# Performance work log

Measured on AMD Instinct MI355X. Metric: run time of the kernel, lower is better.

## Reference

```python
import jax, jax.numpy as jnp
import numpy as np

EPS = 1e-5

def avg_pool3s2(x):
    # AvgPool2d(kernel=3, stride=2, no padding) on NCHW
    s = jax.lax.reduce_window(x, 0.0, jax.lax.add, (1, 1, 3, 3), (1, 1, 2, 2), 'VALID')
    return s / 9.0

def conv1x1(x, W):
    # x: [n,c,h,w], W: [out,c]
    return jnp.einsum('nchw,oc->nohw', x, W)

def batchnorm(x, g, b):
    # training-mode BN over (N,H,W), biased variance (matches torch normalization)
    m = x.mean(axis=(0, 2, 3), keepdims=True)
    v = x.var(axis=(0, 2, 3), keepdims=True)
    return (x - m) * jax.lax.rsqrt(v + EPS) * g[None, :, None, None] + b[None, :, None, None]

def coord_features(hp, wp):
    # [8, hp, wp]: xmin, ymin, xmax, ymax, xctr, yctr, 1/W, 1/H
    w = jnp.arange(wp, dtype=jnp.float32)
    h = jnp.arange(hp, dtype=jnp.float32)
    xmin = w / wp * 2 - 1
    xmax = (w + 1) / wp * 2 - 1
    xctr = (xmin + xmax) / 2
    ymin = h / hp * 2 - 1
    ymax = (h + 1) / hp * 2 - 1
    yctr = (ymin + ymax) / 2
    bx = lambda a: jnp.broadcast_to(a[None, :], (hp, wp))
    by = lambda a: jnp.broadcast_to(a[:, None], (hp, wp))
    const = lambda v: jnp.full((hp, wp), v, dtype=jnp.float32)
    return jnp.stack([bx(xmin), by(ymin), bx(xmax), by(ymax), bx(xctr), by(yctr),
                      const(1.0 / wp), const(1.0 / hp)], axis=0)

def resize_bilinear_ac(x, H, W):
    # bilinear upsample with align_corners=True, x: [n,c,h,w]
    h, w = x.shape[2], x.shape[3]
    ys = jnp.linspace(0.0, h - 1.0, H)
    xs = jnp.linspace(0.0, w - 1.0, W)
    y0 = jnp.floor(ys).astype(jnp.int32); y1 = jnp.minimum(y0 + 1, h - 1); wy = (ys - y0)[None, None, :, None]
    x0 = jnp.floor(xs).astype(jnp.int32); x1 = jnp.minimum(x0 + 1, w - 1); wx = (xs - x0)[None, None, None, :]
    rows = x[:, :, y0, :] * (1 - wy) + x[:, :, y1, :] * wy          # [n,c,H,w]
    return rows[:, :, :, x0] * (1 - wx) + rows[:, :, :, x1] * wx    # [n,c,H,W]

def setup_inputs() -> dict:
    key = jax.random.key(0)
    ks = jax.random.split(key, 8)
    n, in_dim, hid, h, w = 4, 256, 10, 129, 129
    d = hid + 8  # 18
    return {
        'p_fea': jax.random.normal(ks[0], (n, in_dim, h, w), dtype=jnp.float32),
        'hu': jax.random.normal(ks[1], (n, hid, h, w), dtype=jnp.float32),
        'Wq': jax.random.normal(ks[2], (d, d), dtype=jnp.float32) * 0.05,
        'Wk': jax.random.normal(ks[3], (d, in_dim + 8), dtype=jnp.float32) * 0.05,
        'Wv': jax.random.normal(ks[4], (128, in_dim), dtype=jnp.float32) * 0.05,
        'g_v': jnp.ones((128,), dtype=jnp.float32),
        'b_v': jnp.zeros((128,), dtype=jnp.float32),
        'Wp': jax.random.normal(ks[5], (hid, 128), dtype=jnp.float32) * 0.05,
        'g_p': jnp.ones((hid,), dtype=jnp.float32),
        'b_p': jnp.zeros((hid,), dtype=jnp.float32),
    }

def reference(p_fea, hu, Wq, Wk, Wv, g_v, b_v, Wp, g_p, b_p):
    n, c, h, w = p_fea.shape
    p = avg_pool3s2(p_fea)   # [n,256,hp,wp]
    u = avg_pool3s2(hu)      # [n,10,hp,wp]
    hp, wp = p.shape[2], p.shape[3]
    L = hp * wp
    coord = jnp.broadcast_to(coord_features(hp, wp)[None], (n, 8, hp, wp))
    query = conv1x1(jnp.concatenate([u, coord], axis=1), Wq).reshape(n, -1, L).transpose(0, 2, 1)  # [n,L,18]
    key_t = conv1x1(jnp.concatenate([p, coord], axis=1), Wk).reshape(n, -1, L)                      # [n,18,L]
    val = jax.nn.relu(batchnorm(conv1x1(p, Wv), g_v, b_v)).reshape(n, 128, L)                       # [n,128,L]
    energy = jnp.einsum('nlc,ncm->nlm', query, key_t)            # [n,L,L]
    attn = jax.nn.softmax(energy, axis=-1)
    ctx = jnp.einsum('ncm,nlm->ncl', val, attn).reshape(n, 128, hp, wp)
    ctx = jax.nn.relu(batchnorm(conv1x1(ctx, Wp), g_p, b_p))     # [n,10,hp,wp]
    return resize_bilinear_ac(ctx, h, w)                          # [n,10,h,w]
```

## Files before the change

### kernel.cpp

```cpp
#include <hip/hip_runtime.h>
#include <hip/hip_bf16.h>
#include <cstdint>

#define NN   4
#define LL   4096
#define DD   18
#define CVV  128
#define CIN  256
#define CUU  10
#define HH   129
#define COO  10

typedef unsigned short ushort_t;
typedef __attribute__((ext_vector_type(8))) short short8v;
typedef __attribute__((ext_vector_type(4))) short short4v;
typedef __attribute__((ext_vector_type(4))) float f32x4;

#define PB_OFF   ((size_t)0)
#define OP_OFF   ((size_t)2097152)
#define VAL_OFF  ((size_t)2260992)
#define QT_OFF   ((size_t)3309568)
#define KT_OFF   ((size_t)3571712)
#define VT_OFF   ((size_t)3833856)
#define VSC_OFF  ((size_t)4882432)
#define VSH_OFF  ((size_t)4882560)
#define S2_OFF   ((size_t)4882688)
#define SH2_OFF  ((size_t)4882704)
#define PART_OFF ((size_t)4882720)
#define PART2_OFF ((size_t)4915488)
#define KMAX_OFF ((size_t)4916768)

static __device__ __forceinline__ ushort_t f2bf(float x) {
    unsigned int u = __float_as_uint(x);
    unsigned int r = (u + 0x7fffu + ((u >> 16) & 1u)) >> 16;
    return (ushort_t)r;
}
static __device__ __forceinline__ float bf2f(ushort_t b) {
    return __uint_as_float(((unsigned int)b) << 16);
}

static __device__ __forceinline__ void gload16(const void* g, void* l) {
    __builtin_amdgcn_global_load_lds(
        (const __attribute__((address_space(1))) void*)g,
        (__attribute__((address_space(3))) void*)l, 16, 0, 0);
}

__global__ __launch_bounds__(256) void pool_bf_kernel(const float* __restrict__ src,
                                                      ushort_t* __restrict__ dst,
                                                      int* __restrict__ kz) {
    if (kz != nullptr && blockIdx.x == 0 && threadIdx.x < 128) kz[threadIdx.x] = 0;
    int b = blockIdx.x;
    int plane = b >> 4;
    int rg = b & 15;
    __shared__ float rows[9][132];
    const float* sp = src + (size_t)plane * (HH * HH) + (size_t)(rg * 8) * HH;
    #pragma unroll
    for (int j = 0; j < 9; ++j) {
        if (threadIdx.x < HH) rows[j][threadIdx.x] = sp[(size_t)j * HH + threadIdx.x];
    }
    __syncthreads();
    int row = threadIdx.x >> 6, ow = threadIdx.x & 63;
    const float* r0 = rows[2 * row];
    const float* r1 = rows[2 * row + 1];
    const float* r2 = rows[2 * row + 2];
    int x = 2 * ow;
    float sum = r0[x] + r0[x + 1] + r0[x + 2]
              + r1[x] + r1[x + 1] + r1[x + 2]
              + r2[x] + r2[x + 1] + r2[x + 2];
    dst[(size_t)plane * 4096 + (size_t)(rg * 4 + row) * 64 + ow] = f2bf(sum * (1.0f / 9.0f));
}

__global__ __launch_bounds__(256) void qk2f_kernel(const ushort_t* __restrict__ pb,
                                                   const float* __restrict__ hu,
                                                   const float* __restrict__ Wq,
                                                   const float* __restrict__ Wk,
                                                   ushort_t* __restrict__ qt,
                                                   char* __restrict__ kt_c,
                                                   int* __restrict__ kmaxb) {
    int n = blockIdx.x >> 6;
    int mb = blockIdx.x & 63;
    int tid = threadIdx.x;
    int mloc = tid & 63;
    int cs = tid >> 6;
    int m = mb * 64 + mloc;
    int hi = m >> 6, wi = m & 63;

    __shared__ float kacc[4][64][21];

    float coord[8];
    coord[0] = wi * (2.0f / 64.0f) - 1.0f;
    coord[1] = hi * (2.0f / 64.0f) - 1.0f;
    coord[2] = (wi + 1) * (2.0f / 64.0f) - 1.0f;
    coord[3] = (hi + 1) * (2.0f / 64.0f) - 1.0f;
    coord[4] = 0.5f * (coord[0] + coord[2]);
    coord[5] = 0.5f * (coord[1] + coord[3]);
    coord[6] = 1.0f / 64.0f;
    coord[7] = 1.0f / 64.0f;

    {
        float acc[DD];
        #pragma unroll
        for (int o = 0; o < DD; ++o) acc[o] = 0.0f;
        const ushort_t* pc = pb + ((size_t)(n * CIN + cs * 64)) * LL + m;
        for (int c0 = 0; c0 < 64; ++c0) {
            float pv = bf2f(pc[(size_t)c0 * LL]);
            const float* wr = Wk + (cs * 64 + c0);
            #pragma unroll
            for (int o = 0; o < DD; ++o) acc[o] = fmaf(pv, wr[o * 264], acc[o]);
        }
        if (cs == 3) {
            #pragma unroll
            for (int j = 0; j < 8; ++j) {
                float cv = coord[j];
                #pragma unroll
                for (int o = 0; o < DD; ++o) acc[o] = fmaf(cv, Wk[o * 264 + CIN + j], acc[o]);
            }
        }
        #pragma unroll
        for (int o = 0; o < DD; ++o) kacc[cs][mloc][o] = acc[o];
    }
    if (cs == 0) {
        float acc[DD];
        #pragma unroll
        for (int o = 0; o < DD; ++o) acc[o] = 0.0f;
        const float* hub = hu + ((size_t)(n * CUU)) * (HH * HH) + (size_t)(2 * hi) * HH + 2 * wi;
        for (int cq = 0; cq < CUU; ++cq) {
            const float* s = hub + (size_t)cq * (HH * HH);
            float uv = (s[0] + s[1] + s[2]
                      + s[HH] + s[HH + 1] + s[HH + 2]
                      + s[2 * HH] + s[2 * HH + 1] + s[2 * HH + 2]) * (1.0f / 9.0f);
            #pragma unroll
            for (int o = 0; o < DD; ++o) acc[o] = fmaf(uv, Wq[o * DD + cq], acc[o]);
        }
        #pragma unroll
        for (int j = 0; j < 8; ++j) {
            float cv = coord[j];
            #pragma unroll
            for (int o = 0; o < DD; ++o) acc[o] = fmaf(cv, Wq[o * DD + CUU + j], acc[o]);
        }
        union { short8v v[4]; ushort_t s[32]; } pk;
        #pragma unroll
        for (int o = 0; o < 32; ++o) pk.s[o] = (o < DD) ? f2bf(acc[o]) : (ushort_t)0;
        short8v* qrow = (short8v*)(qt + ((size_t)(n * LL) + m) * 32);
        #pragma unroll
        for (int j = 0; j < 4; ++j) qrow[j] = pk.v[j];
    }
    __syncthreads();
    {
        int j = cs;
        union { short8v v; ushort_t s[8]; } pk;
        #pragma unroll
        for (int i = 0; i < 8; ++i) {
            int o = j * 8 + i;
            float v = 0.0f;
            if (o < DD)
                v = kacc[0][mloc][o] + kacc[1][mloc][o] + kacc[2][mloc][o] + kacc[3][mloc][o];
            pk.s[i] = (o < DD) ? f2bf(v) : (ushort_t)0;
        }
        int byte = ((mloc << 6) | (j << 4)) ^ (((mloc >> 1) & 7) << 4);
        *(short8v*)(kt_c + (size_t)n * 262144 + (size_t)mb * 4096 + byte) = pk.v;

        int mb8[8];
        #pragma unroll
        for (int i = 0; i < 8; ++i) mb8[i] = (int)(pk.s[i] & 0x7fffu);
        #pragma unroll
        for (int off = 1; off < 64; off <<= 1) {
            #pragma unroll
            for (int i = 0; i < 8; ++i) {
                int ov = __shfl_xor(mb8[i], off);
                mb8[i] = max(mb8[i], ov);
            }
        }
        if (mloc == 0) {
            #pragma unroll
            for (int i = 0; i < 8; ++i)
                atomicMax(&kmaxb[n * 32 + cs * 8 + i], mb8[i] << 16);
        }
    }
}

__global__ __launch_bounds__(256, 2) void val_gemm3_kernel(const ushort_t* __restrict__ pb,
                                                           const float* __restrict__ Wv,
                                                           ushort_t* __restrict__ val,
                                                           float* __restrict__ part) {
    int b = blockIdx.x;
    int n  = b >> 7;
    int cb = (b >> 5) & 3;
    int mb = b & 31;
    int tid = threadIdx.x;
    int cg = tid >> 5;
    int mg = tid & 31;
    int ch0 = cb * 32;
    int m0 = mb * 128;

    __shared__ float Wt[256][36];

    {
        int c4 = tid & 63;
        int chq = tid >> 6;
        #pragma unroll
        for (int j = 0; j < 8; ++j) {
            int ch = chq * 8 + j;
            float4 v = *(const float4*)&Wv[(size_t)(ch0 + ch) * CIN + c4 * 4];
            Wt[c4 * 4 + 0][ch] = v.x;
            Wt[c4 * 4 + 1][ch] = v.y;
            Wt[c4 * 4 + 2][ch] = v.z;
            Wt[c4 * 4 + 3][ch] = v.w;
        }
    }
    __syncthreads();

    const ushort_t* pbb = pb + (size_t)n * CIN * LL + m0 + mg * 4;
    f32x4 a0 = {0.f,0.f,0.f,0.f}, a1 = {0.f,0.f,0.f,0.f};
    f32x4 a2 = {0.f,0.f,0.f,0.f}, a3 = {0.f,0.f,0.f,0.f};

    #pragma unroll 4
    for (int c = 0; c < CIN; ++c) {
        short4v ps = *(const short4v*)(pbb + (size_t)c * LL);
        f32x4 pv;
        pv[0] = bf2f((ushort_t)ps[0]); pv[1] = bf2f((ushort_t)ps[1]);
        pv[2] = bf2f((ushort_t)ps[2]); pv[3] = bf2f((ushort_t)ps[3]);
        f32x4 wv = *(const f32x4*)&Wt[c][cg * 4];
        a0 += pv * wv.x;
        a1 += pv * wv.y;
        a2 += pv * wv.z;
        a3 += pv * wv.w;
    }

    size_t out = ((size_t)(n * CVV + ch0 + cg * 4)) * LL + m0 + mg * 4;
    union { short4v v; ushort_t s[4]; } w0, w1, w2, w3;
    #pragma unroll
    for (int i = 0; i < 4; ++i) {
        w0.s[i] = f2bf(a0[i]); w1.s[i] = f2bf(a1[i]);
        w2.s[i] = f2bf(a2[i]); w3.s[i] = f2bf(a3[i]);
    }
    *(short4v*)&val[out]          = w0.v;
    *(short4v*)&val[out + LL]     = w1.v;
    *(short4v*)&val[out + 2*LL]   = w2.v;
    *(short4v*)&val[out + 3*LL]   = w3.v;

    float s1[4], s2[4];
    s1[0] = a0[0]+a0[1]+a0[2]+a0[3]; s2[0] = a0[0]*a0[0]+a0[1]*a0[1]+a0[2]*a0[2]+a0[3]*a0[3];
    s1[1] = a1[0]+a1[1]+a1[2]+a1[3]; s2[1] = a1[0]*a1[0]+a1[1]*a1[1]+a1[2]*a1[2]+a1[3]*a1[3];
    s1[2] = a2[0]+a2[1]+a2[2]+a2[3]; s2[2] = a2[0]*a2[0]+a2[1]*a2[1]+a2[2]*a2[2]+a2[3]*a2[3];
    s1[3] = a3[0]+a3[1]+a3[2]+a3[3]; s2[3] = a3[0]*a3[0]+a3[1]*a3[1]+a3[2]*a3[2]+a3[3]*a3[3];
    #pragma unroll
    for (int off = 1; off < 32; off <<= 1) {
        #pragma unroll
        for (int i = 0; i < 4; ++i) {
            s1[i] += __shfl_xor(s1[i], off);
            s2[i] += __shfl_xor(s2[i], off);
        }
    }
    if (mg == 0) {
        #pragma unroll
        for (int i = 0; i < 4; ++i) {
            part[(((size_t)b * 8 + cg) * 4 + i) * 2]     = s1[i];
            part[(((size_t)b * 8 + cg) * 4 + i) * 2 + 1] = s2[i];
        }
    }
}

__global__ __launch_bounds__(128) void bn_finalize_v_kernel(const float* __restrict__ part,
                                                            const float* __restrict__ g,
                                                            const float* __restrict__ bta,
                                                            float* __restrict__ scale,
                                                            float* __restrict__ shift) {
    int ch = threadIdx.x;
    if (ch >= CVV) return;
    int cb = ch >> 5;
    int cg = (ch & 31) >> 2;
    int i = ch & 3;
    float s1 = 0.0f, s2 = 0.0f;
    for (int n = 0; n < NN; ++n) {
        for (int mb = 0; mb < 32; ++mb) {
            int b = n * 128 + cb * 32 + mb;
            size_t idx = (((size_t)b * 8 + cg) * 4 + i) * 2;
            s1 += part[idx];
            s2 += part[idx + 1];
        }
    }
    float mean = s1 * (1.0f / (NN * LL));
    float var = s2 * (1.0f / (NN * LL)) - mean * mean;
    float inv = rsqrtf(var + 1e-5f);
    float sc = g[ch] * inv;
    scale[ch] = sc;
    shift[ch] = bta[ch] - mean * sc;
}

__global__ __launch_bounds__(256) void bn_apply2_kernel(const ushort_t* __restrict__ val,
                                                        const float* __restrict__ scale,
                                                        const float* __restrict__ shift,
                                                        char* __restrict__ vt_c) {
    int t = blockIdx.x * 256 + threadIdx.x;
    int mq = t & 511;
    int ch = (t >> 9) & 127;
    int n = t >> 16;
    int m0 = mq * 8;
    short8v vs = *(const short8v*)(val + ((size_t)(n * CVV + ch)) * LL + m0);
    float sc = scale[ch], sh = shift[ch];
    union { short8v v; ushort_t s[8]; } pk;
    #pragma unroll
    for (int i = 0; i < 8; ++i)
        pk.s[i] = f2bf(fmaxf(fmaf(bf2f((ushort_t)vs[i]), sc, sh), 0.0f));
    int tile = m0 >> 6, mloc = m0 & 63;
    size_t byte = (size_t)n * 1048576 + (size_t)tile * 16384
                + (size_t)(((ch << 7) | (mloc << 1)) ^ ((ch & 7) << 4));
    *(short8v*)(vt_c + byte) = pk.v;
}

struct PW { ushort_t p[16][72]; };

__global__ __launch_bounds__(256, 2) void attn_proj_kernel(const ushort_t* __restrict__ qt,
                                                           const char* __restrict__ kt_c,
                                                           const char* __restrict__ vt_c,
                                                           const int* __restrict__ kmaxb,
                                                           const float* __restrict__ Wp,
                                                           float* __restrict__ ypart,
                                                           float* __restrict__ Lp) {
    int orig = blockIdx.x;
    int bid = ((orig & 7) << 6) | (orig >> 3);
    int qb = bid & 63;
    int sM = (bid >> 6) & 1;
    int n = bid >> 7;
    int tid = threadIdx.x;
    int w = tid >> 6, lane = tid & 63, c = lane & 15, g = lane >> 4;
    int l0w = qb * 64 + w * 16;

    __shared__ __align__(16) ushort_t K_t[2][2048];
    __shared__ __align__(16) ushort_t V_t[2][8192];
    __shared__ PW pws[4];
    __shared__ float Wpl[COO][CVV];

    for (int i = tid; i < COO * CVV; i += 256) Wpl[i >> 7][i & 127] = Wp[i];

    const char* ktb = kt_c + (size_t)n * 262144;
    const char* vtb = vt_c + (size_t)n * 1048576;
    int tk64 = sM * 32;

    short8v qf = *(const short8v*)(qt + (((size_t)n * LL + l0w + c) << 5) + g * 8);
    int vxor = (c & 7) << 4;

    float bound = 0.0f;
    {
        const int* km = kmaxb + n * 32 + g * 8;
        #pragma unroll
        for (int i = 0; i < 8; ++i) {
            float kv = __int_as_float(km[i]);
            float aq = __uint_as_float(((unsigned int)((ushort_t)qf[i]) & 0x7fffu) << 16);
            bound = fmaf(aq, kv, bound);
        }
        bound += __shfl_xor(bound, 16);
        bound += __shfl_xor(bound, 32);
    }
    float M[4];
    #pragma unroll
    for (int r = 0; r < 4; ++r) M[r] = __shfl(bound, g * 4 + r);

    f32x4 O[8];
    #pragma unroll
    for (int i = 0; i < 8; ++i) O[i] = (f32x4){0.f, 0.f, 0.f, 0.f};
    float Lacc[4] = {0.f, 0.f, 0.f, 0.f};

    {
        const char* ks = ktb + (size_t)tk64 * 4096 + w * 1024 + lane * 16;
        gload16(ks, (char*)K_t[0] + w * 1024);
        const char* vs = vtb + (size_t)tk64 * 16384 + w * 4096 + lane * 16;
        #pragma unroll
        for (int i = 0; i < 4; ++i)
            gload16(vs + i * 1024, (char*)V_t[0] + w * 4096 + i * 1024);
    }
    __syncthreads();
    int buf = 0;
    for (int mt = 0; mt < 32; ++mt) {
        if (mt + 1 < 32) {
            const char* ks = ktb + (size_t)(tk64 + mt + 1) * 4096 + w * 1024 + lane * 16;
            gload16(ks, (char*)K_t[buf ^ 1] + w * 1024);
            const char* vs = vtb + (size_t)(tk64 + mt + 1) * 16384 + w * 4096 + lane * 16;
            #pragma unroll
            for (int i = 0; i < 4; ++i)
                gload16(vs + i * 1024, (char*)V_t[buf ^ 1] + w * 4096 + i * 1024);
        }
        f32x4 S[4];
        const char* kb = (const char*)K_t[buf];
        #pragma unroll
        for (int t = 0; t < 4; ++t) {
            int krow = t * 16 + c;
            int kby = ((krow << 6) | (g << 4)) ^ (((krow >> 1) & 7) << 4);
            short8v kf = *(const short8v*)(kb + kby);
            S[t] = __builtin_amdgcn_mfma_f32_16x16x32_bf16(qf, kf, (f32x4){0.f, 0.f, 0.f, 0.f}, 0, 0, 0);
        }
        #pragma unroll
        for (int t = 0; t < 4; ++t) {
            #pragma unroll
            for (int r = 0; r < 4; ++r) {
                float pv = __expf(S[t][r] - M[r]);
                Lacc[r] += pv;
                pws[w].p[g * 4 + r][t * 16 + c] = f2bf(pv);
            }
        }
        short8v pa0 = *(const short8v*)&pws[w].p[c][g * 8];
        short8v pa1 = *(const short8v*)&pws[w].p[c][32 + g * 8];
        const char* vb = (const char*)V_t[buf];
        __builtin_amdgcn_s_setprio(1);
        #pragma unroll
        for (int ct = 0; ct < 8; ++ct) {
            int row = ct * 16 + c;
            int vby0 = (row << 7) | ((g << 4) ^ vxor);
            int vby1 = (row << 7) | (((1 << 6) | (g << 4)) ^ vxor);
            short8v v0 = *(const short8v*)(vb + vby0);
            short8v v1 = *(const short8v*)(vb + vby1);
            O[ct] = __builtin_amdgcn_mfma_f32_16x16x32_bf16(pa0, v0, O[ct], 0, 0, 0);
            O[ct] = __builtin_amdgcn_mfma_f32_16x16x32_bf16(pa1, v1, O[ct], 0, 0, 0);
        }
        __builtin_amdgcn_s_setprio(0);
        __syncthreads();
        buf ^= 1;
    }
    #pragma unroll
    for (int off = 1; off < 16; off <<= 1) {
        #pragma unroll
        for (int r = 0; r < 4; ++r) Lacc[r] += __shfl_xor(Lacc[r], off);
    }

    float yp[COO][4];
    #pragma unroll
    for (int o = 0; o < COO; ++o)
        #pragma unroll
        for (int r = 0; r < 4; ++r) yp[o][r] = 0.0f;
    #pragma unroll
    for (int ct = 0; ct < 8; ++ct) {
        #pragma unroll
        for (int o = 0; o < COO; ++o) {
            float wv = Wpl[o][ct * 16 + c];
            #pragma unroll
            for (int r = 0; r < 4; ++r)
                yp[o][r] = fmaf(O[ct][r], wv, yp[o][r]);
        }
    }
    #pragma unroll
    for (int off = 1; off < 16; off <<= 1) {
        #pragma unroll
        for (int o = 0; o < COO; ++o)
            #pragma unroll
            for (int r = 0; r < 4; ++r)
                yp[o][r] += __shfl_xor(yp[o][r], off);
    }
    if (c == 0) {
        #pragma unroll
        for (int r = 0; r < 4; ++r) {
            size_t yrow = (size_t)(sM * (NN * LL) + n * LL + l0w + g * 4 + r);
            #pragma unroll
            for (int o = 0; o < COO; ++o)
                ypart[yrow * COO + o] = yp[o][r];
            Lp[yrow] = Lacc[r];
        }
    }
}

__global__ __launch_bounds__(256) void combine2b_kernel(const float* __restrict__ ypart,
                                                        const float* __restrict__ Lp,
                                                        float* __restrict__ out_pre,
                                                        float* __restrict__ part2) {
    int idx = blockIdx.x * 256 + threadIdx.x;
    int n = idx >> 12;
    int l = idx & 4095;
    int nl = n * LL + l;
    float inv = 1.0f / (Lp[nl] + Lp[NN * LL + nl]);
    const float* y0 = ypart + (size_t)nl * COO;
    const float* y1 = ypart + ((size_t)(NN * LL) + nl) * COO;
    float ov[COO];
    #pragma unroll
    for (int o = 0; o < COO; ++o) {
        ov[o] = (y0[o] + y1[o]) * inv;
        out_pre[((size_t)(n * COO + o)) * LL + l] = ov[o];
    }
    float p1[COO], p2[COO];
    #pragma unroll
    for (int o = 0; o < COO; ++o) { p1[o] = ov[o]; p2[o] = ov[o] * ov[o]; }
    #pragma unroll
    for (int off = 1; off < 64; off <<= 1) {
        #pragma unroll
        for (int o = 0; o < COO; ++o) {
            p1[o] += __shfl_xor(p1[o], off);
            p2[o] += __shfl_xor(p2[o], off);
        }
    }
    __shared__ float rs1[4][COO], rs2[4][COO];
    int w = threadIdx.x >> 6, lane = threadIdx.x & 63;
    if (lane == 0) {
        #pragma unroll
        for (int o = 0; o < COO; ++o) { rs1[w][o] = p1[o]; rs2[w][o] = p2[o]; }
    }
    __syncthreads();
    if (threadIdx.x < COO) {
        int o = threadIdx.x;
        float a = rs1[0][o] + rs1[1][o] + rs1[2][o] + rs1[3][o];
        float b = rs2[0][o] + rs2[1][o] + rs2[2][o] + rs2[3][o];
        part2[((size_t)blockIdx.x * COO + o) * 2]     = a;
        part2[((size_t)blockIdx.x * COO + o) * 2 + 1] = b;
    }
}

__global__ __launch_bounds__(64) void bn_finalize2_kernel(const float* __restrict__ part2,
                                                          const float* __restrict__ g,
                                                          const float* __restrict__ bta,
                                                          float* __restrict__ scale,
                                                          float* __restrict__ shift) {
    int ch = threadIdx.x;
    if (ch >= COO) return;
    float s1 = 0.0f, s2 = 0.0f;
    for (int b = 0; b < 64; ++b) {
        s1 += part2[((size_t)b * COO + ch) * 2];
        s2 += part2[((size_t)b * COO + ch) * 2 + 1];
    }
    float mean = s1 * (1.0f / (NN * LL));
    float var = s2 * (1.0f / (NN * LL)) - mean * mean;
    float inv = rsqrtf(var + 1e-5f);
    float sc = g[ch] * inv;
    scale[ch] = sc;
    shift[ch] = bta[ch] - mean * sc;
}

__global__ __launch_bounds__(256) void resize_kernel(const float* __restrict__ out_pre,
                                                     const float* __restrict__ scale,
                                                     const float* __restrict__ shift,
                                                     float* __restrict__ out,
                                                     int total) {
    int idx = blockIdx.x * 256 + threadIdx.x;
    if (idx >= total) return;
    int ow = idx % HH;
    int t = idx / HH;
    int oh = t % HH;
    int t2 = t / HH;
    int o = t2 % COO;
    int n = t2 / COO;

    const float r = 63.0f / 128.0f;
    float y = oh * r;
    float x = ow * r;
    int y0 = (int)y;
    int x0 = (int)x;
    float wy = y - y0;
    float wx = x - x0;
    int y1 = min(y0 + 1, 63);
    int x1 = min(x0 + 1, 63);

    const float* base = out_pre + ((size_t)(n * COO + o)) * LL;
    float sc = scale[o], sh = shift[o];
    float v00 = fmaxf(fmaf(base[y0 * 64 + x0], sc, sh), 0.0f);
    float v01 = fmaxf(fmaf(base[y0 * 64 + x1], sc, sh), 0.0f);
    float v10 = fmaxf(fmaf(base[y1 * 64 + x0], sc, sh), 0.0f);
    float v11 = fmaxf(fmaf(base[y1 * 64 + x1], sc, sh), 0.0f);
    float top = v00 * (1.0f - wx) + v01 * wx;
    float bot = v10 * (1.0f - wx) + v11 * wx;
    out[idx] = top * (1.0f - wy) + bot * wy;
}

extern "C" void kernel_launch(void* const* d_in, const int* in_sizes, int n_in,
                              void* d_out, int out_size, void* d_ws, size_t ws_size,
                              hipStream_t stream) {
    (void)in_sizes; (void)n_in; (void)out_size; (void)ws_size;
    const float* p_fea = (const float*)d_in[0];
    const float* hu    = (const float*)d_in[1];
    const float* Wq    = (const float*)d_in[2];
    const float* Wk    = (const float*)d_in[3];
    const float* Wv    = (const float*)d_in[4];
    const float* g_v   = (const float*)d_in[5];
    const float* b_v   = (const float*)d_in[6];
    const float* Wp    = (const float*)d_in[7];
    const float* g_p   = (const float*)d_in[8];
    const float* b_p   = (const float*)d_in[9];

    float* ws = (float*)d_ws;
    ushort_t* pbb     = (ushort_t*)(ws + PB_OFF);
    float*    out_pre = ws + OP_OFF;
    ushort_t* valb    = (ushort_t*)(ws + VAL_OFF);
    ushort_t* qtb     = (ushort_t*)(ws + QT_OFF);
    char*     ktb     = (char*)(ws + KT_OFF);
    char*     vtb     = (char*)(ws + VT_OFF);
    float*    Lpart   = ws + VAL_OFF;
    float*    ypart   = ws + VAL_OFF + 32768;
    float*    vscale  = ws + VSC_OFF;
    float*    vshift  = ws + VSH_OFF;
    float*    scale2  = ws + S2_OFF;
    float*    shift2  = ws + SH2_OFF;
    float*    part    = ws + PART_OFF;
    float*    part2   = ws + PART2_OFF;
    int*      kmaxb   = (int*)(ws + KMAX_OFF);

    pool_bf_kernel<<<NN * CIN * 16, 256, 0, stream>>>(p_fea, pbb, kmaxb);
    qk2f_kernel<<<256, 256, 0, stream>>>(pbb, hu, Wq, Wk, qtb, ktb, kmaxb);
    val_gemm3_kernel<<<512, 256, 0, stream>>>(pbb, Wv, valb, part);
    bn_finalize_v_kernel<<<1, 128, 0, stream>>>(part, g_v, b_v, vscale, vshift);
    bn_apply2_kernel<<<(NN * CVV * 512) / 256, 256, 0, stream>>>(valb, vscale, vshift, vtb);
    attn_proj_kernel<<<512, 256, 0, stream>>>(qtb, ktb, vtb, kmaxb, Wp, ypart, Lpart);
    combine2b_kernel<<<(NN * LL) / 256, 256, 0, stream>>>(ypart, Lpart, out_pre, part2);
    bn_finalize2_kernel<<<1, 64, 0, stream>>>(part2, g_p, b_p, scale2, shift2);
    {
        int total = NN * COO * HH * HH;
        resize_kernel<<<(total + 255) / 256, 256, 0, stream>>>(out_pre, scale2, shift2,
                                                               (float*)d_out, total);
    }
}
```

Measured before the change: 155.4 us.

## Fuse QK and value GEMM launches, restructure attention to swapped MFMA with 4-way key split

```diff
diff --git a/kernel.cpp b/kernel.cpp
--- a/kernel.cpp
+++ b/kernel.cpp
@@ -38,6 +38,9 @@
 static __device__ __forceinline__ float bf2f(ushort_t b) {
     return __uint_as_float(((unsigned int)b) << 16);
 }
+static __device__ __forceinline__ unsigned int pk2(float a, float b) {
+    return (unsigned int)f2bf(a) | ((unsigned int)f2bf(b) << 16);
+}
 
 static __device__ __forceinline__ void gload16(const void* g, void* l) {
     __builtin_amdgcn_global_load_lds(
@@ -70,193 +73,192 @@
     dst[(size_t)plane * 4096 + (size_t)(rg * 4 + row) * 64 + ow] = f2bf(sum * (1.0f / 9.0f));
 }
 
-__global__ __launch_bounds__(256) void qk2f_kernel(const ushort_t* __restrict__ pb,
-                                                   const float* __restrict__ hu,
-                                                   const float* __restrict__ Wq,
-                                                   const float* __restrict__ Wk,
-                                                   ushort_t* __restrict__ qt,
-                                                   char* __restrict__ kt_c,
-                                                   int* __restrict__ kmaxb) {
-    int n = blockIdx.x >> 6;
-    int mb = blockIdx.x & 63;
+__global__ __launch_bounds__(256, 2) void qkval_kernel(const ushort_t* __restrict__ pb,
+                                                       const float* __restrict__ hu,
+                                                       const float* __restrict__ Wq,
+                                                       const float* __restrict__ Wk,
+                                                       const float* __restrict__ Wv,
+                                                       ushort_t* __restrict__ qt,
+                                                       char* __restrict__ kt_c,
+                                                       int* __restrict__ kmaxb,
+                                                       ushort_t* __restrict__ val,
+                                                       float* __restrict__ part) {
+    __shared__ __align__(16) char smem[36864];
     int tid = threadIdx.x;
-    int mloc = tid & 63;
-    int cs = tid >> 6;
-    int m = mb * 64 + mloc;
-    int hi = m >> 6, wi = m & 63;
-
-    __shared__ float kacc[4][64][21];
-
-    float coord[8];
-    coord[0] = wi * (2.0f / 64.0f) - 1.0f;
-    coord[1] = hi * (2.0f / 64.0f) - 1.0f;
-    coord[2] = (wi + 1) * (2.0f / 64.0f) - 1.0f;
-    coord[3] = (hi + 1) * (2.0f / 64.0f) - 1.0f;
-    coord[4] = 0.5f * (coord[0] + coord[2]);
-    coord[5] = 0.5f * (coord[1] + coord[3]);
-    coord[6] = 1.0f / 64.0f;
-    coord[7] = 1.0f / 64.0f;
-
-    {
-        float acc[DD];
-        #pragma unroll
-        for (int o = 0; o < DD; ++o) acc[o] = 0.0f;
-        const ushort_t* pc = pb + ((size_t)(n * CIN + cs * 64)) * LL + m;
-        for (int c0 = 0; c0 < 64; ++c0) {
-            float pv = bf2f(pc[(size_t)c0 * LL]);
-            const float* wr = Wk + (cs * 64 + c0);
-            #pragma unroll
-            for (int o = 0; o < DD; ++o) acc[o] = fmaf(pv, wr[o * 264], acc[o]);
-        }
-        if (cs == 3) {
+
+    if (blockIdx.x < 256) {
+        float (*kacc)[64][21] = (float(*)[64][21])smem;
+        int n = blockIdx.x >> 6;
+        int mb = blockIdx.x & 63;
+        int mloc = tid & 63;
+        int cs = tid >> 6;
+        int m = mb * 64 + mloc;
+        int hi = m >> 6, wi = m & 63;
+
+        float coord[8];
+        coord[0] = wi * (2.0f / 64.0f) - 1.0f;
+        coord[1] = hi * (2.0f / 64.0f) - 1.0f;
+        coord[2] = (wi + 1) * (2.0f / 64.0f) - 1.0f;
+        coord[3] = (hi + 1) * (2.0f / 64.0f) - 1.0f;
+        coord[4] = 0.5f * (coord[0] + coord[2]);
+        coord[5] = 0.5f * (coord[1] + coord[3]);
+        coord[6] = 1.0f / 64.0f;
+        coord[7] = 1.0f / 64.0f;
+
+        {
+            float acc[DD];
+            #pragma unroll
+            for (int o = 0; o < DD; ++o) acc[o] = 0.0f;
+            const ushort_t* pc = pb + ((size_t)(n * CIN + cs * 64)) * LL + m;
+            for (int c0 = 0; c0 < 64; ++c0) {
+                float pv = bf2f(pc[(size_t)c0 * LL]);
+                const float* wr = Wk + (cs * 64 + c0);
+                #pragma unroll
+                for (int o = 0; o < DD; ++o) acc[o] = fmaf(pv, wr[o * 264], acc[o]);
+            }
+            if (cs == 3) {
+                #pragma unroll
+                for (int j = 0; j < 8; ++j) {
+                    float cv = coord[j];
+                    #pragma unroll
+                    for (int o = 0; o < DD; ++o) acc[o] = fmaf(cv, Wk[o * 264 + CIN + j], acc[o]);
+                }
+            }
+            #pragma unroll
+            for (int o = 0; o < DD; ++o) kacc[cs][mloc][o] = acc[o];
+        }
+        if (cs == 0) {
+            float acc[DD];
+            #pragma unroll
+            for (int o = 0; o < DD; ++o) acc[o] = 0.0f;
+            const float* hub = hu + ((size_t)(n * CUU)) * (HH * HH) + (size_t)(2 * hi) * HH + 2 * wi;
+            for (int cq = 0; cq < CUU; ++cq) {
+                const float* s = hub + (size_t)cq * (HH * HH);
+                float uv = (s[0] + s[1] + s[2]
+                          + s[HH] + s[HH + 1] + s[HH + 2]
+                          + s[2 * HH] + s[2 * HH + 1] + s[2 * HH + 2]) * (1.0f / 9.0f);
+                #pragma unroll
+                for (int o = 0; o < DD; ++o) acc[o] = fmaf(uv, Wq[o * DD + cq], acc[o]);
+            }
             #pragma unroll
             for (int j = 0; j < 8; ++j) {
                 float cv = coord[j];
                 #pragma unroll
-                for (int o = 0; o < DD; ++o) acc[o] = fmaf(cv, Wk[o * 264 + CIN + j], acc[o]);
-            }
-        }
-        #pragma unroll
-        for (int o = 0; o < DD; ++o) kacc[cs][mloc][o] = acc[o];
-    }
-    if (cs == 0) {
-        float acc[DD];
-        #pragma unroll
-        for (int o = 0; o < DD; ++o) acc[o] = 0.0f;
-        const float* hub = hu + ((size_t)(n * CUU)) * (HH * HH) + (size_t)(2 * hi) * HH + 2 * wi;
-        for (int cq = 0; cq < CUU; ++cq) {
-            const float* s = hub + (size_t)cq * (HH * HH);
-            float uv = (s[0] + s[1] + s[2]
-                      + s[HH] + s[HH + 1] + s[HH + 2]
-                      + s[2 * HH] + s[2 * HH + 1] + s[2 * HH + 2]) * (1.0f / 9.0f);
-            #pragma unroll
-            for (int o = 0; o < DD; ++o) acc[o] = fmaf(uv, Wq[o * DD + cq], acc[o]);
-        }
-        #pragma unroll
-        for (int j = 0; j < 8; ++j) {
-            float cv = coord[j];
-            #pragma unroll
-            for (int o = 0; o < DD; ++o) acc[o] = fmaf(cv, Wq[o * DD + CUU + j], acc[o]);
-        }
-        union { short8v v[4]; ushort_t s[32]; } pk;
-        #pragma unroll
-        for (int o = 0; o < 32; ++o) pk.s[o] = (o < DD) ? f2bf(acc[o]) : (ushort_t)0;
-        short8v* qrow = (short8v*)(qt + ((size_t)(n * LL) + m) * 32);
-        #pragma unroll
-        for (int j = 0; j < 4; ++j) qrow[j] = pk.v[j];
-    }
-    __syncthreads();
-    {
-        int j = cs;
-        union { short8v v; ushort_t s[8]; } pk;
-        #pragma unroll
-        for (int i = 0; i < 8; ++i) {
-            int o = j * 8 + i;
-            float v = 0.0f;
-            if (o < DD)
-                v = kacc[0][mloc][o] + kacc[1][mloc][o] + kacc[2][mloc][o] + kacc[3][mloc][o];
-            pk.s[i] = (o < DD) ? f2bf(v) : (ushort_t)0;
-        }
-        int byte = ((mloc << 6) | (j << 4)) ^ (((mloc >> 1) & 7) << 4);
-        *(short8v*)(kt_c + (size_t)n * 262144 + (size_t)mb * 4096 + byte) = pk.v;
-
-        int mb8[8];
-        #pragma unroll
-        for (int i = 0; i < 8; ++i) mb8[i] = (int)(pk.s[i] & 0x7fffu);
-        #pragma unroll
-        for (int off = 1; off < 64; off <<= 1) {
+                for (int o = 0; o < DD; ++o) acc[o] = fmaf(cv, Wq[o * DD + CUU + j], acc[o]);
+            }
+            union { short8v v[4]; ushort_t s[32]; } pk;
+            #pragma unroll
+            for (int o = 0; o < 32; ++o) pk.s[o] = (o < DD) ? f2bf(acc[o]) : (ushort_t)0;
+            short8v* qrow = (short8v*)(qt + ((size_t)(n * LL) + m) * 32);
+            #pragma unroll
+            for (int j = 0; j < 4; ++j) qrow[j] = pk.v[j];
+        }
+        __syncthreads();
+        {
+            int j = cs;
+            union { short8v v; ushort_t s[8]; } pk;
             #pragma unroll
             for (int i = 0; i < 8; ++i) {
-                int ov = __shfl_xor(mb8[i], off);
-                mb8[i] = max(mb8[i], ov);
-            }
-        }
-        if (mloc == 0) {
-            #pragma unroll
-            for (int i = 0; i < 8; ++i)
-                atomicMax(&kmaxb[n * 32 + cs * 8 + i], mb8[i] << 16);
-        }
-    }
-}
-
-__global__ __launch_bounds__(256, 2) void val_gemm3_kernel(const ushort_t* __restrict__ pb,
-                                                           const float* __restrict__ Wv,
-                                                           ushort_t* __restrict__ val,
-                                                           float* __restrict__ part) {
-    int b = blockIdx.x;
-    int n  = b >> 7;
-    int cb = (b >> 5) & 3;
-    int mb = b & 31;
-    int tid = threadIdx.x;
-    int cg = tid >> 5;
-    int mg = tid & 31;
-    int ch0 = cb * 32;
-    int m0 = mb * 128;
-
-    __shared__ float Wt[256][36];
-
-    {
-        int c4 = tid & 63;
-        int chq = tid >> 6;
-        #pragma unroll
-        for (int j = 0; j < 8; ++j) {
-            int ch = chq * 8 + j;
-            float4 v = *(const float4*)&Wv[(size_t)(ch0 + ch) * CIN + c4 * 4];
-            Wt[c4 * 4 + 0][ch] = v.x;
-            Wt[c4 * 4 + 1][ch] = v.y;
-            Wt[c4 * 4 + 2][ch] = v.z;
-            Wt[c4 * 4 + 3][ch] = v.w;
-        }
-    }
-    __syncthreads();
-
-    const ushort_t* pbb = pb + (size_t)n * CIN * LL + m0 + mg * 4;
-    f32x4 a0 = {0.f,0.f,0.f,0.f}, a1 = {0.f,0.f,0.f,0.f};
-    f32x4 a2 = {0.f,0.f,0.f,0.f}, a3 = {0.f,0.f,0.f,0.f};
-
-    #pragma unroll 4
-    for (int c = 0; c < CIN; ++c) {
-        short4v ps = *(const short4v*)(pbb + (size_t)c * LL);
-        f32x4 pv;
-        pv[0] = bf2f((ushort_t)ps[0]); pv[1] = bf2f((ushort_t)ps[1]);
-        pv[2] = bf2f((ushort_t)ps[2]); pv[3] = bf2f((ushort_t)ps[3]);
-        f32x4 wv = *(const f32x4*)&Wt[c][cg * 4];
-        a0 += pv * wv.x;
-        a1 += pv * wv.y;
-        a2 += pv * wv.z;
-        a3 += pv * wv.w;
-    }
-
-    size_t out = ((size_t)(n * CVV + ch0 + cg * 4)) * LL + m0 + mg * 4;
-    union { short4v v; ushort_t s[4]; } w0, w1, w2, w3;
-    #pragma unroll
-    for (int i = 0; i < 4; ++i) {
-        w0.s[i] = f2bf(a0[i]); w1.s[i] = f2bf(a1[i]);
-        w2.s[i] = f2bf(a2[i]); w3.s[i] = f2bf(a3[i]);
-    }
-    *(short4v*)&val[out]          = w0.v;
-    *(short4v*)&val[out + LL]     = w1.v;
-    *(short4v*)&val[out + 2*LL]   = w2.v;
-    *(short4v*)&val[out + 3*LL]   = w3.v;
-
-    float s1[4], s2[4];
-    s1[0] = a0[0]+a0[1]+a0[2]+a0[3]; s2[0] = a0[0]*a0[0]+a0[1]*a0[1]+a0[2]*a0[2]+a0[3]*a0[3];
-    s1[1] = a1[0]+a1[1]+a1[2]+a1[3]; s2[1] = a1[0]*a1[0]+a1[1]*a1[1]+a1[2]*a1[2]+a1[3]*a1[3];
-    s1[2] = a2[0]+a2[1]+a2[2]+a2[3]; s2[2] = a2[0]*a2[0]+a2[1]*a2[1]+a2[2]*a2[2]+a2[3]*a2[3];
-    s1[3] = a3[0]+a3[1]+a3[2]+a3[3]; s2[3] = a3[0]*a3[0]+a3[1]*a3[1]+a3[2]*a3[2]+a3[3]*a3[3];
-    #pragma unroll
-    for (int off = 1; off < 32; off <<= 1) {
+                int o = j * 8 + i;
+                float v = 0.0f;
+                if (o < DD)
+                    v = kacc[0][mloc][o] + kacc[1][mloc][o] + kacc[2][mloc][o] + kacc[3][mloc][o];
+                pk.s[i] = (o < DD) ? f2bf(v) : (ushort_t)0;
+            }
+            int byte = ((mloc << 6) | (j << 4)) ^ (((mloc >> 1) & 7) << 4);
+            *(short8v*)(kt_c + (size_t)n * 262144 + (size_t)mb * 4096 + byte) = pk.v;
+
+            int mb8[8];
+            #pragma unroll
+            for (int i = 0; i < 8; ++i) mb8[i] = (int)(pk.s[i] & 0x7fffu);
+            #pragma unroll
+            for (int off = 1; off < 64; off <<= 1) {
+                #pragma unroll
+                for (int i = 0; i < 8; ++i) {
+                    int ov = __shfl_xor(mb8[i], off);
+                    mb8[i] = max(mb8[i], ov);
+                }
+            }
+            if (mloc == 0) {
+                #pragma unroll
+                for (int i = 0; i < 8; ++i)
+                    atomicMax(&kmaxb[n * 32 + cs * 8 + i], mb8[i] << 16);
+            }
+        }
+    } else {
+        float (*Wt)[36] = (float(*)[36])smem;
+        int b = blockIdx.x - 256;
+        int n  = b >> 7;
+        int cb = (b >> 5) & 3;
+        int mb = b & 31;
+        int cg = tid >> 5;
+        int mg = tid & 31;
+        int ch0 = cb * 32;
+        int m0 = mb * 128;
+
+        {
+            int c4 = tid & 63;
+            int chq = tid >> 6;
+            #pragma unroll
+            for (int j = 0; j < 8; ++j) {
+                int ch = chq * 8 + j;
+                float4 v = *(const float4*)&Wv[(size_t)(ch0 + ch) * CIN + c4 * 4];
+                Wt[c4 * 4 + 0][ch] = v.x;
+                Wt[c4 * 4 + 1][ch] = v.y;
+                Wt[c4 * 4 + 2][ch] = v.z;
+                Wt[c4 * 4 + 3][ch] = v.w;
+            }
+        }
+        __syncthreads();
+
+        const ushort_t* pbb = pb + (size_t)n * CIN * LL + m0 + mg * 4;
+        f32x4 a0 = {0.f,0.f,0.f,0.f}, a1 = {0.f,0.f,0.f,0.f};
+        f32x4 a2 = {0.f,0.f,0.f,0.f}, a3 = {0.f,0.f,0.f,0.f};
+
+        #pragma unroll 4
+        for (int c = 0; c < CIN; ++c) {
+            short4v ps = *(const short4v*)(pbb + (size_t)c * LL);
+            f32x4 pv;
+            pv[0] = bf2f((ushort_t)ps[0]); pv[1] = bf2f((ushort_t)ps[1]);
+            pv[2] = bf2f((ushort_t)ps[2]); pv[3] = bf2f((ushort_t)ps[3]);
+            f32x4 wv = *(const f32x4*)&Wt[c][cg * 4];
+            a0 += pv * wv.x;
+            a1 += pv * wv.y;
+            a2 += pv * wv.z;
+            a3 += pv * wv.w;
+        }
+
+        size_t out = ((size_t)(n * CVV + ch0 + cg * 4)) * LL + m0 + mg * 4;
+        union { short4v v; ushort_t s[4]; } w0, w1, w2, w3;
         #pragma unroll
         for (int i = 0; i < 4; ++i) {
-            s1[i] += __shfl_xor(s1[i], off);
-            s2[i] += __shfl_xor(s2[i], off);
-        }
-    }
-    if (mg == 0) {
-        #pragma unroll
-        for (int i = 0; i < 4; ++i) {
-            part[(((size_t)b * 8 + cg) * 4 + i) * 2]     = s1[i];
-            part[(((size_t)b * 8 + cg) * 4 + i) * 2 + 1] = s2[i];
+            w0.s[i] = f2bf(a0[i]); w1.s[i] = f2bf(a1[i]);
+            w2.s[i] = f2bf(a2[i]); w3.s[i] = f2bf(a3[i]);
+        }
+        *(short4v*)&val[out]          = w0.v;
+        *(short4v*)&val[out + LL]     = w1.v;
+        *(short4v*)&val[out + 2*LL]   = w2.v;
+        *(short4v*)&val[out + 3*LL]   = w3.v;
+
+        float s1[4], s2[4];
+        s1[0] = a0[0]+a0[1]+a0[2]+a0[3]; s2[0] = a0[0]*a0[0]+a0[1]*a0[1]+a0[2]*a0[2]+a0[3]*a0[3];
+        s1[1] = a1[0]+a1[1]+a1[2]+a1[3]; s2[1] = a1[0]*a1[0]+a1[1]*a1[1]+a1[2]*a1[2]+a1[3]*a1[3];
+        s1[2] = a2[0]+a2[1]+a2[2]+a2[3]; s2[2] = a2[0]*a2[0]+a2[1]*a2[1]+a2[2]*a2[2]+a2[3]*a2[3];
+        s1[3] = a3[0]+a3[1]+a3[2]+a3[3]; s2[3] = a3[0]*a3[0]+a3[1]*a3[1]+a3[2]*a3[2]+a3[3]*a3[3];
+        #pragma unroll
+        for (int off = 1; off < 32; off <<= 1) {
+            #pragma unroll
+            for (int i = 0; i < 4; ++i) {
+                s1[i] += __shfl_xor(s1[i], off);
+                s2[i] += __shfl_xor(s2[i], off);
+            }
+        }
+        if (mg == 0) {
+            #pragma unroll
+            for (int i = 0; i < 4; ++i) {
+                part[(((size_t)b * 8 + cg) * 4 + i) * 2]     = s1[i];
+                part[(((size_t)b * 8 + cg) * 4 + i) * 2 + 1] = s2[i];
+            }
         }
     }
 }
@@ -303,125 +305,126 @@
     #pragma unroll
     for (int i = 0; i < 8; ++i)
         pk.s[i] = f2bf(fmaxf(fmaf(bf2f((ushort_t)vs[i]), sc, sh), 0.0f));
-    int tile = m0 >> 6, mloc = m0 & 63;
-    size_t byte = (size_t)n * 1048576 + (size_t)tile * 16384
-                + (size_t)(((ch << 7) | (mloc << 1)) ^ ((ch & 7) << 4));
+    int tile = m0 >> 5, mloc = m0 & 31;
+    size_t byte = (size_t)n * 1048576 + (size_t)tile * 8192
+                + (size_t)(((ch << 6) | (mloc << 1)) ^ ((ch & 7) << 4));
     *(short8v*)(vt_c + byte) = pk.v;
 }
 
-struct PW { ushort_t p[16][72]; };
-
-__global__ __launch_bounds__(256, 2) void attn_proj_kernel(const ushort_t* __restrict__ qt,
-                                                           const char* __restrict__ kt_c,
-                                                           const char* __restrict__ vt_c,
-                                                           const int* __restrict__ kmaxb,
-                                                           const float* __restrict__ Wp,
-                                                           float* __restrict__ ypart,
-                                                           float* __restrict__ Lp) {
+__global__ __launch_bounds__(256, 4) void attn_swz_kernel(const ushort_t* __restrict__ qt,
+                                                          const char* __restrict__ kt_c,
+                                                          const char* __restrict__ vt_c,
+                                                          const int* __restrict__ kmaxb,
+                                                          const float* __restrict__ Wp,
+                                                          float* __restrict__ ypart,
+                                                          float* __restrict__ Lp) {
     int orig = blockIdx.x;
-    int bid = ((orig & 7) << 6) | (orig >> 3);
-    int qb = bid & 63;
-    int sM = (bid >> 6) & 1;
-    int n = bid >> 7;
+    int xcd = orig & 7;
+    int idx = orig >> 3;
+    int qb = idx >> 1;
+    int combo = xcd * 2 + (idx & 1);
+    int n = combo >> 2;
+    int sM = combo & 3;
+    int T0 = sM * 32;
+
     int tid = threadIdx.x;
     int w = tid >> 6, lane = tid & 63, c = lane & 15, g = lane >> 4;
     int l0w = qb * 64 + w * 16;
 
-    __shared__ __align__(16) ushort_t K_t[2][2048];
-    __shared__ __align__(16) ushort_t V_t[2][8192];
-    __shared__ PW pws[4];
+    __shared__ __align__(16) ushort_t K_t[2][1024];
+    __shared__ __align__(16) ushort_t V_t[2][4096];
+    __shared__ __align__(16) uint4 exch[4][64];
     __shared__ float Wpl[COO][CVV];
 
     for (int i = tid; i < COO * CVV; i += 256) Wpl[i >> 7][i & 127] = Wp[i];
 
     const char* ktb = kt_c + (size_t)n * 262144;
     const char* vtb = vt_c + (size_t)n * 1048576;
-    int tk64 = sM * 32;
 
     short8v qf = *(const short8v*)(qt + (((size_t)n * LL + l0w + c) << 5) + g * 8);
     int vxor = (c & 7) << 4;
 
-    float bound = 0.0f;
+    float Mq = 0.0f;
     {
         const int* km = kmaxb + n * 32 + g * 8;
         #pragma unroll
         for (int i = 0; i < 8; ++i) {
             float kv = __int_as_float(km[i]);
             float aq = __uint_as_float(((unsigned int)((ushort_t)qf[i]) & 0x7fffu) << 16);
-            bound = fmaf(aq, kv, bound);
-        }
-        bound += __shfl_xor(bound, 16);
-        bound += __shfl_xor(bound, 32);
-    }
-    float M[4];
-    #pragma unroll
-    for (int r = 0; r < 4; ++r) M[r] = __shfl(bound, g * 4 + r);
+            Mq = fmaf(aq, kv, Mq);
+        }
+        Mq += __shfl_xor(Mq, 16);
+        Mq += __shfl_xor(Mq, 32);
+    }
 
     f32x4 O[8];
     #pragma unroll
     for (int i = 0; i < 8; ++i) O[i] = (f32x4){0.f, 0.f, 0.f, 0.f};
-    float Lacc[4] = {0.f, 0.f, 0.f, 0.f};
-
+    float Lacc = 0.0f;
+
+    int kby0, kby1;
     {
-        const char* ks = ktb + (size_t)tk64 * 4096 + w * 1024 + lane * 16;
-        gload16(ks, (char*)K_t[0] + w * 1024);
-        const char* vs = vtb + (size_t)tk64 * 16384 + w * 4096 + lane * 16;
-        #pragma unroll
-        for (int i = 0; i < 4; ++i)
-            gload16(vs + i * 1024, (char*)V_t[0] + w * 4096 + i * 1024);
+        int kr0 = c, kr1 = 16 + c;
+        kby0 = ((kr0 << 6) | (g << 4)) ^ (((kr0 >> 1) & 7) << 4);
+        kby1 = ((kr1 << 6) | (g << 4)) ^ (((kr1 >> 1) & 7) << 4);
+    }
+    int srcA = ((g & 1) << 5) + c;
+    int toff = (g >> 1) * 8;
+
+    {
+        int T = T0;
+        const char* ks = ktb + (size_t)(T >> 1) * 4096 + (T & 1) * 2048 + w * 1024 + lane * 16;
+        if (w < 2) gload16(ks, (char*)K_t[0] + w * 1024);
+        const char* vs = vtb + (size_t)T * 8192 + w * 2048 + lane * 16;
+        gload16(vs, (char*)V_t[0] + w * 2048);
+        gload16(vs + 1024, (char*)V_t[0] + w * 2048 + 1024);
     }
     __syncthreads();
     int buf = 0;
     for (int mt = 0; mt < 32; ++mt) {
         if (mt + 1 < 32) {
-            const char* ks = ktb + (size_t)(tk64 + mt + 1) * 4096 + w * 1024 + lane * 16;
-            gload16(ks, (char*)K_t[buf ^ 1] + w * 1024);
-            const char* vs = vtb + (size_t)(tk64 + mt + 1) * 16384 + w * 4096 + lane * 16;
-            #pragma unroll
-            for (int i = 0; i < 4; ++i)
-                gload16(vs + i * 1024, (char*)V_t[buf ^ 1] + w * 4096 + i * 1024);
-        }
-        f32x4 S[4];
+            int T = T0 + mt + 1;
+            const char* ks = ktb + (size_t)(T >> 1) * 4096 + (T & 1) * 2048 + w * 1024 + lane * 16;
+            if (w < 2) gload16(ks, (char*)K_t[buf ^ 1] + w * 1024);
+            const char* vs = vtb + (size_t)T * 8192 + w * 2048 + lane * 16;
+            gload16(vs, (char*)V_t[buf ^ 1] + w * 2048);
+            gload16(vs + 1024, (char*)V_t[buf ^ 1] + w * 2048 + 1024);
+        }
         const char* kb = (const char*)K_t[buf];
-        #pragma unroll
-        for (int t = 0; t < 4; ++t) {
-            int krow = t * 16 + c;
-            int kby = ((krow << 6) | (g << 4)) ^ (((krow >> 1) & 7) << 4);
-            short8v kf = *(const short8v*)(kb + kby);
-            S[t] = __builtin_amdgcn_mfma_f32_16x16x32_bf16(qf, kf, (f32x4){0.f, 0.f, 0.f, 0.f}, 0, 0, 0);
-        }
-        #pragma unroll
-        for (int t = 0; t < 4; ++t) {
-            #pragma unroll
-            for (int r = 0; r < 4; ++r) {
-                float pv = __expf(S[t][r] - M[r]);
-                Lacc[r] += pv;
-                pws[w].p[g * 4 + r][t * 16 + c] = f2bf(pv);
-            }
-        }
-        short8v pa0 = *(const short8v*)&pws[w].p[c][g * 8];
-        short8v pa1 = *(const short8v*)&pws[w].p[c][32 + g * 8];
+        short8v kf0 = *(const short8v*)(kb + kby0);
+        short8v kf1 = *(const short8v*)(kb + kby1);
+        f32x4 S0 = __builtin_amdgcn_mfma_f32_16x16x32_bf16(kf0, qf, (f32x4){0.f,0.f,0.f,0.f}, 0, 0, 0);
+        f32x4 S1 = __builtin_amdgcn_mfma_f32_16x16x32_bf16(kf1, qf, (f32x4){0.f,0.f,0.f,0.f}, 0, 0, 0);
+        float p0[4], p1[4];
+        #pragma unroll
+        for (int r = 0; r < 4; ++r) {
+            p0[r] = __expf(S0[r] - Mq);
+            p1[r] = __expf(S1[r] - Mq);
+            Lacc += p0[r] + p1[r];
+        }
+        exch[w][lane] = (uint4){ pk2(p0[0], p0[1]), pk2(p0[2], p0[3]),
+                                 pk2(p1[0], p1[1]), pk2(p1[2], p1[3]) };
+        const char* eb = (const char*)&exch[w][0];
+        uint2 ua = *(const uint2*)(eb + srcA * 16 + toff);
+        uint2 ub = *(const uint2*)(eb + (srcA + 16) * 16 + toff);
+        union { unsigned int u[4]; short8v v; } pa;
+        pa.u[0] = ua.x; pa.u[1] = ua.y; pa.u[2] = ub.x; pa.u[3] = ub.y;
         const char* vb = (const char*)V_t[buf];
         __builtin_amdgcn_s_setprio(1);
         #pragma unroll
         for (int ct = 0; ct < 8; ++ct) {
-            int row = ct * 16 + c;
-            int vby0 = (row << 7) | ((g << 4) ^ vxor);
-            int vby1 = (row << 7) | (((1 << 6) | (g << 4)) ^ vxor);
-            short8v v0 = *(const short8v*)(vb + vby0);
-            short8v v1 = *(const short8v*)(vb + vby1);
-            O[ct] = __builtin_amdgcn_mfma_f32_16x16x32_bf16(pa0, v0, O[ct], 0, 0, 0);
-            O[ct] = __builtin_amdgcn_mfma_f32_16x16x32_bf16(pa1, v1, O[ct], 0, 0, 0);
+            int vby = (((ct * 16 + c) << 6) | (g << 4)) ^ vxor;
+            short8v vf = *(const short8v*)(vb + vby);
+            O[ct] = __builtin_amdgcn_mfma_f32_16x16x32_bf16(pa.v, vf, O[ct], 0, 0, 0);
         }
         __builtin_amdgcn_s_setprio(0);
         __syncthreads();
         buf ^= 1;
     }
-    #pragma unroll
-    for (int off = 1; off < 16; off <<= 1) {
-        #pragma unroll
-        for (int r = 0; r < 4; ++r) Lacc[r] += __shfl_xor(Lacc[r], off);
-    }
+    Lacc += __shfl_xor(Lacc, 16);
+    Lacc += __shfl_xor(Lacc, 32);
+    if (g == 0)
+        Lp[sM * (NN * LL) + n * LL + l0w + c] = Lacc;
 
     float yp[COO][4];
     #pragma unroll
@@ -453,12 +456,11 @@
             #pragma unroll
             for (int o = 0; o < COO; ++o)
                 ypart[yrow * COO + o] = yp[o][r];
-            Lp[yrow] = Lacc[r];
-        }
-    }
-}
-
-__global__ __launch_bounds__(256) void combine2b_kernel(const float* __restrict__ ypart,
+        }
+    }
+}
+
+__global__ __launch_bounds__(256) void combine4b_kernel(const float* __restrict__ ypart,
                                                         const float* __restrict__ Lp,
                                                         float* __restrict__ out_pre,
                                                         float* __restrict__ part2) {
@@ -466,13 +468,15 @@
     int n = idx >> 12;
     int l = idx & 4095;
     int nl = n * LL + l;
-    float inv = 1.0f / (Lp[nl] + Lp[NN * LL + nl]);
+    float inv = 1.0f / (Lp[nl] + Lp[16384 + nl] + Lp[2 * 16384 + nl] + Lp[3 * 16384 + nl]);
     const float* y0 = ypart + (size_t)nl * COO;
-    const float* y1 = ypart + ((size_t)(NN * LL) + nl) * COO;
+    const float* y1 = ypart + ((size_t)16384 + nl) * COO;
+    const float* y2 = ypart + ((size_t)(2 * 16384) + nl) * COO;
+    const float* y3 = ypart + ((size_t)(3 * 16384) + nl) * COO;
     float ov[COO];
     #pragma unroll
     for (int o = 0; o < COO; ++o) {
-        ov[o] = (y0[o] + y1[o]) * inv;
+        ov[o] = (y0[o] + y1[o] + y2[o] + y3[o]) * inv;
         out_pre[((size_t)(n * COO + o)) * LL + l] = ov[o];
     }
     float p1[COO], p2[COO];
@@ -580,7 +584,7 @@
     char*     ktb     = (char*)(ws + KT_OFF);
     char*     vtb     = (char*)(ws + VT_OFF);
     float*    Lpart   = ws + VAL_OFF;
-    float*    ypart   = ws + VAL_OFF + 32768;
+    float*    ypart   = ws + VAL_OFF + 65536;
     float*    vscale  = ws + VSC_OFF;
     float*    vshift  = ws + VSH_OFF;
     float*    scale2  = ws + S2_OFF;
@@ -590,12 +594,11 @@
     int*      kmaxb   = (int*)(ws + KMAX_OFF);
 
     pool_bf_kernel<<<NN * CIN * 16, 256, 0, stream>>>(p_fea, pbb, kmaxb);
-    qk2f_kernel<<<256, 256, 0, stream>>>(pbb, hu, Wq, Wk, qtb, ktb, kmaxb);
-    val_gemm3_kernel<<<512, 256, 0, stream>>>(pbb, Wv, valb, part);
+    qkval_kernel<<<768, 256, 0, stream>>>(pbb, hu, Wq, Wk, Wv, qtb, ktb, kmaxb, valb, part);
     bn_finalize_v_kernel<<<1, 128, 0, stream>>>(part, g_v, b_v, vscale, vshift);
     bn_apply2_kernel<<<(NN * CVV * 512) / 256, 256, 0, stream>>>(valb, vscale, vshift, vtb);
-    attn_proj_kernel<<<512, 256, 0, stream>>>(qtb, ktb, vtb, kmaxb, Wp, ypart, Lpart);
-    combine2b_kernel<<<(NN * LL) / 256, 256, 0, stream>>>(ypart, Lpart, out_pre, part2);
+    attn_swz_kernel<<<1024, 256, 0, stream>>>(qtb, ktb, vtb, kmaxb, Wp, ypart, Lpart);
+    combine4b_kernel<<<(NN * LL) / 256, 256, 0, stream>>>(ypart, Lpart, out_pre, part2);
     bn_finalize2_kernel<<<1, 64, 0, stream>>>(part2, g_p, b_p, scale2, shift2);
     {
         int total = NN * COO * HH * HH;
```

Result: faster. 140.5 us (-9.6%).
